# Performance work log

Hardware: AMD Instinct MI355X
Metric: run time of the kernel (lower is better)

Reference implementation:

```python
import jax, jax.numpy as jnp
import numpy as np

D_MODEL = 1024
D_FF = 4096
N_EXPERTS = 8
THRESHOLD = 0.8
EPS = 1e-6


def setup_inputs() -> dict:
    key = jax.random.key(0)
    ks = jax.random.split(key, 8)
    x = jax.random.normal(ks[0], (2, 1024, D_MODEL), jnp.float32)
    Wg = jax.random.normal(ks[1], (D_MODEL, N_EXPERTS), jnp.float32) * (D_MODEL ** -0.5)
    bg = jnp.zeros((N_EXPERTS,), jnp.float32)
    W1 = jax.random.normal(ks[2], (N_EXPERTS, D_MODEL, D_FF), jnp.float32) * (D_MODEL ** -0.5)
    b1 = jnp.zeros((N_EXPERTS, D_FF), jnp.float32)
    W3 = jax.random.normal(ks[3], (N_EXPERTS, D_MODEL, D_FF), jnp.float32) * (D_MODEL ** -0.5)
    b3 = jnp.zeros((N_EXPERTS, D_FF), jnp.float32)
    W2 = jax.random.normal(ks[4], (N_EXPERTS, D_FF, D_MODEL), jnp.float32) * (D_FF ** -0.5)
    b2 = jnp.zeros((N_EXPERTS, D_MODEL), jnp.float32)
    return {"x": x, "Wg": Wg, "bg": bg, "W1": W1, "b1": b1, "W3": W3, "b3": b3, "W2": W2, "b2": b2}


def _route(x, Wg, bg):
    # Dynamic-K (top-p) router
    logits = x @ Wg + bg                                  # [B,S,E]
    probs = jax.nn.softmax(logits, axis=-1)
    order = jnp.argsort(-probs, axis=-1)                  # descending sort indices
    sp = jnp.take_along_axis(probs, order, axis=-1)       # sorted probs
    shifted = jnp.cumsum(sp, axis=-1) - sp                # exclusive cumsum
    active = shifted < THRESHOLD
    active = active.at[..., 0].set(True)                  # always keep top-1
    ap = sp * active.astype(sp.dtype)
    aw = ap / (ap.sum(axis=-1, keepdims=True) + EPS)      # renormalized weights
    inv = jnp.argsort(order, axis=-1)                     # scatter == gather by inverse perm
    weights = jnp.take_along_axis(aw, inv, axis=-1)       # [B,S,E] in expert order
    return weights, probs, active.sum(axis=-1)


def reference(x, Wg, bg, W1, b1, W3, b3, W2, b2):
    B, S, D = x.shape
    E = W1.shape[0]
    weights, probs, active_count = _route(x, Wg, bg)
    xf = x.reshape(-1, D)                                 # [T,D]
    wf = weights.reshape(-1, E)                           # [T,E]
    # Dense grouped SwiGLU experts; zero routing weight zeroes the contribution,
    # matching the masked gather/scatter math of the original.
    h = jnp.einsum('td,edf->etf', xf, W1) + b1[:, None, :]
    g = jax.nn.silu(h) * (jnp.einsum('td,edf->etf', xf, W3) + b3[:, None, :])
    out_e = jnp.einsum('etf,efd->etd', g, W2) + b2[:, None, :]
    final = jnp.einsum('etd,te->td', out_e, wf).reshape(B, S, D)
    # auxiliary losses
    f_i = (wf > 0).astype(x.dtype).mean(axis=0)           # fraction of tokens per expert
    P_i = probs.reshape(-1, E).mean(axis=0)               # mean router prob per expert
    loss_balance = E * jnp.sum(f_i * P_i)
    loss_entropy = (-jnp.sum(probs * jnp.log(probs + EPS), axis=-1)).mean()
    return final, loss_balance, loss_entropy, active_count
```

## Files before the change

### kernel.cpp

```cpp
#include <hip/hip_runtime.h>
#include <hip/hip_bf16.h>
#include <math.h>

#define D_MODEL 1024
#define D_FF    4096
#define N_EXP   8
#define TOKENS  2048
#define THRESH  0.8f
#define EPS_R   1e-6f

#define FINAL_SIZE (TOKENS * D_MODEL)

typedef unsigned short ushort_t;
typedef __attribute__((ext_vector_type(4))) float f32x4;
typedef __attribute__((ext_vector_type(8))) short bf16x8;
typedef __attribute__((ext_vector_type(8))) unsigned short ushort8_t;

__device__ __forceinline__ unsigned short f2bf(float f) {
    unsigned u = __builtin_bit_cast(unsigned, f);
    unsigned r = (u + 0x7FFFu + ((u >> 16) & 1u)) >> 16;
    return (unsigned short)r;
}
__device__ __forceinline__ float bf2f(unsigned short b) {
    unsigned u = ((unsigned)b) << 16;
    return __builtin_bit_cast(float, u);
}

template <typename T>
__device__ __forceinline__ void gload16(const T* gsrc, T* ldst) {
    __builtin_amdgcn_global_load_lds((const __attribute__((address_space(1))) unsigned int*)gsrc,
                                     (__attribute__((address_space(3))) unsigned int*)ldst,
                                     16, 0, 0);
}

#define VMCNT4() asm volatile("s_waitcnt vmcnt(4)" ::: "memory")
#define VMCNT0() asm volatile("s_waitcnt vmcnt(0)" ::: "memory")
#define BAR()    do { __builtin_amdgcn_s_barrier(); asm volatile("" ::: "memory"); } while (0)

__global__ __launch_bounds__(256) void convert_x_kernel(const float* __restrict__ x,
                                                        ushort_t* __restrict__ xbf) {
    int i = blockIdx.x * 256 + threadIdx.x;
    const float4 v = reinterpret_cast<const float4*>(x)[i];
    ushort4 o;
    o.x = f2bf(v.x); o.y = f2bf(v.y); o.z = f2bf(v.z); o.w = f2bf(v.w);
    reinterpret_cast<ushort4*>(xbf)[i] = o;
}

__global__ __launch_bounds__(256) void wconv_all_kernel(const float* __restrict__ W1,
                                                        const float* __restrict__ W3,
                                                        const float* __restrict__ W2,
                                                        ushort_t* __restrict__ w1t,
                                                        ushort_t* __restrict__ w3t,
                                                        ushort_t* __restrict__ w2t) {
    __shared__ float sT[64][65];
    const int idx = blockIdx.x;
    const int sel = idx >> 13;
    const int r = idx & 8191;
    int K, N, k0, n0, e;
    const float* src;
    ushort_t* dst;
    if (sel < 2) {
        K = D_MODEL; N = D_FF;
        n0 = (r & 63) * 64;
        k0 = ((r >> 6) & 15) * 64;
        e = r >> 10;
        src = (sel == 0 ? W1 : W3) + (size_t)e * K * N;
        dst = (sel == 0 ? w1t : w3t) + (size_t)e * K * N;
    } else {
        K = D_FF; N = D_MODEL;
        n0 = (r & 15) * 64;
        k0 = ((r >> 4) & 63) * 64;
        e = r >> 10;
        src = W2 + (size_t)e * K * N;
        dst = w2t + (size_t)e * K * N;
    }
    const int t = threadIdx.x;
    {
        const int k = t >> 2;
        const int c = (t & 3) * 16;
        const float* s = src + (size_t)(k0 + k) * N + n0 + c;
#pragma unroll
        for (int j = 0; j < 4; ++j) {
            float4 v = *reinterpret_cast<const float4*>(s + 4 * j);
            sT[k][c + 4 * j + 0] = v.x; sT[k][c + 4 * j + 1] = v.y;
            sT[k][c + 4 * j + 2] = v.z; sT[k][c + 4 * j + 3] = v.w;
        }
    }
    __syncthreads();
    {
        const int n = t >> 2;
        const int ks = (t & 3) * 16;
        ushort_t* d = dst + (size_t)(n0 + n) * K + k0 + ks;
#pragma unroll
        for (int h = 0; h < 2; ++h) {
            ushort8_t o;
#pragma unroll
            for (int j = 0; j < 8; ++j) o[j] = f2bf(sT[ks + h * 8 + j][n]);
            *reinterpret_cast<ushort8_t*>(d + h * 8) = o;
        }
    }
}

__global__ __launch_bounds__(256) void router_kernel(const float* __restrict__ x,
                                                     const float* __restrict__ Wg,
                                                     const float* __restrict__ bg,
                                                     float* __restrict__ wts,
                                                     float* __restrict__ probs,
                                                     float* __restrict__ ent,
                                                     float* __restrict__ act_out)
{
    int wave = threadIdx.x >> 6;
    int lane = threadIdx.x & 63;
    int t = blockIdx.x * 4 + wave;

    float acc[8];
#pragma unroll
    for (int e = 0; e < 8; ++e) acc[e] = 0.f;

    const float* xrow = x + (size_t)t * D_MODEL;
    for (int d = lane; d < D_MODEL; d += 64) {
        float xv = xrow[d];
        const float4* wg = reinterpret_cast<const float4*>(Wg + (size_t)d * 8);
        float4 a = wg[0], b = wg[1];
        acc[0] += xv * a.x; acc[1] += xv * a.y; acc[2] += xv * a.z; acc[3] += xv * a.w;
        acc[4] += xv * b.x; acc[5] += xv * b.y; acc[6] += xv * b.z; acc[7] += xv * b.w;
    }
#pragma unroll
    for (int e = 0; e < 8; ++e) {
#pragma unroll
        for (int off = 32; off > 0; off >>= 1) acc[e] += __shfl_xor(acc[e], off);
    }

    if (lane == 0) {
        float l[8], p[8];
        float m = -1e30f;
#pragma unroll
        for (int e = 0; e < 8; ++e) { l[e] = acc[e] + bg[e]; m = fmaxf(m, l[e]); }
        float s = 0.f;
#pragma unroll
        for (int e = 0; e < 8; ++e) { p[e] = expf(l[e] - m); s += p[e]; }
        float inv = 1.f / s;
#pragma unroll
        for (int e = 0; e < 8; ++e) p[e] *= inv;

        int idx[8]; float sp[8];
#pragma unroll
        for (int e = 0; e < 8; ++e) { idx[e] = e; sp[e] = p[e]; }
        for (int i = 0; i < 8; ++i) {
            int best = i;
            for (int j = i + 1; j < 8; ++j) if (sp[j] > sp[best]) best = j;
            float tv = sp[i]; sp[i] = sp[best]; sp[best] = tv;
            int ti = idx[i]; idx[i] = idx[best]; idx[best] = ti;
        }
        float cum = 0.f, asum = 0.f, ap[8];
        int cnt = 0;
        for (int i = 0; i < 8; ++i) {
            int active = (i == 0) || (cum < THRESH);
            cum += sp[i];
            ap[i] = active ? sp[i] : 0.f;
            asum += ap[i];
            cnt += active;
        }
        float rinv = 1.f / (asum + EPS_R);
        float w[8];
        for (int i = 0; i < 8; ++i) w[idx[i]] = ap[i] * rinv;

        float* wrow = wts + (size_t)t * 8;
        float* prow = probs + (size_t)t * 8;
        float e_sum = 0.f;
#pragma unroll
        for (int e = 0; e < 8; ++e) {
            wrow[e] = w[e];
            prow[e] = p[e];
            e_sum -= p[e] * logf(p[e] + EPS_R);
        }
        ent[t] = e_sum;
        act_out[t] = (float)cnt;
    }
}

__global__ __launch_bounds__(512) void build_lists_kernel(const float* __restrict__ wts,
                                                          int* __restrict__ tok,
                                                          int* __restrict__ pos,
                                                          int* __restrict__ cnt) {
    const int e = threadIdx.x >> 6;
    const int lane = threadIdx.x & 63;
    int base = 0;
    for (int t0 = 0; t0 < TOKENS; t0 += 64) {
        int t = t0 + lane;
        float w = wts[(size_t)t * 8 + e];
        unsigned long long mask = __ballot(w > 0.f);
        int rank = __popcll(mask & ((1ull << lane) - 1ull));
        if (w > 0.f) {
            tok[e * TOKENS + base + rank] = t;
            pos[(size_t)t * 8 + e] = base + rank;
        } else {
            pos[(size_t)t * 8 + e] = -1;
        }
        base += __popcll(mask);
    }
    if (lane == 0) cnt[e] = base;
}

__global__ __launch_bounds__(256) void loss_kernel(const float* __restrict__ wts,
                                                   const float* __restrict__ probs,
                                                   const float* __restrict__ ent,
                                                   float* __restrict__ out_scalars)
{
    const int tid = threadIdx.x;
    const int lane = tid & 63;
    const int wv = tid >> 6;
    float fsum[8], psum[8], es = 0.f;
#pragma unroll
    for (int e = 0; e < 8; ++e) { fsum[e] = 0.f; psum[e] = 0.f; }
    for (int t = tid; t < TOKENS; t += 256) {
        const float* wrow = wts + (size_t)t * 8;
        const float* prow = probs + (size_t)t * 8;
#pragma unroll
        for (int e = 0; e < 8; ++e) {
            fsum[e] += (wrow[e] > 0.f) ? 1.f : 0.f;
            psum[e] += prow[e];
        }
        es += ent[t];
    }
#pragma unroll
    for (int e = 0; e < 8; ++e) {
#pragma unroll
        for (int off = 32; off > 0; off >>= 1) {
            fsum[e] += __shfl_xor(fsum[e], off);
            psum[e] += __shfl_xor(psum[e], off);
        }
    }
#pragma unroll
    for (int off = 32; off > 0; off >>= 1) es += __shfl_xor(es, off);

    __shared__ float red[4][17];
    if (lane == 0) {
#pragma unroll
        for (int e = 0; e < 8; ++e) { red[wv][e] = fsum[e]; red[wv][8 + e] = psum[e]; }
        red[wv][16] = es;
    }
    __syncthreads();
    if (tid == 0) {
        float tot[17];
#pragma unroll
        for (int q = 0; q < 17; ++q) tot[q] = red[0][q] + red[1][q] + red[2][q] + red[3][q];
        const float invT = 1.f / (float)TOKENS;
        float lb = 0.f;
        for (int e = 0; e < 8; ++e) lb += (tot[e] * invT) * (tot[8 + e] * invT);
        out_scalars[0] = 8.f * lb;
        out_scalars[1] = tot[16] * invT;
    }
}

__global__ __launch_bounds__(256, 2) void gemm1_kernel(const ushort_t* __restrict__ xbf,
                                                       const ushort_t* __restrict__ w1t,
                                                       const ushort_t* __restrict__ w3t,
                                                       const float* __restrict__ b1,
                                                       const float* __restrict__ b3,
                                                       const int* __restrict__ tok,
                                                       const int* __restrict__ cnts,
                                                       ushort_t* __restrict__ g,
                                                       int gbase) {
    const int z = blockIdx.z;
    const int ge = gbase + z;
    const int cnt = cnts[ge];

    const int NX = D_FF / 64;
    const int CHUNK = NX / 8;
    const int orig = blockIdx.x + NX * blockIdx.y;
    const int inner = orig >> 3;
    const int nx = (orig & 7) * CHUNK + (inner & (CHUNK - 1));
    const int ny = inner / CHUNK;
    const int m0 = ny * 128;
    const int n0 = nx * 64;
    if (m0 >= cnt) return;

    __shared__ ushort_t sA0[128 * 32], sA1[128 * 32];
    __shared__ ushort_t sB10[64 * 32], sB11[64 * 32];
    __shared__ ushort_t sB30[64 * 32], sB31[64 * 32];

    const int tid = threadIdx.x;
    const int lane = tid & 63;
    const int wave = tid >> 6;
    const int wr = wave >> 1, wc = wave & 1;

    f32x4 acc1[4][2], acc3[4][2];
#pragma unroll
    for (int i = 0; i < 4; ++i)
#pragma unroll
        for (int j = 0; j < 2; ++j) { acc1[i][j] = (f32x4)0.f; acc3[i][j] = (f32x4)0.f; }

    const int srow = tid >> 2;
    const int scol = (tid & 3) * 8;

    const ushort_t* abase[2];
#pragma unroll
    for (int r = 0; r < 2; ++r) {
        int i = m0 + srow + r * 64;
        i = (i < cnt) ? i : (cnt - 1);
        abase[r] = xbf + (size_t)tok[ge * TOKENS + i] * D_MODEL + scol;
    }
    const ushort_t* w1p = w1t + (size_t)z * D_FF * D_MODEL + (size_t)(n0 + srow) * D_MODEL + scol;
    const ushort_t* w3p = w3t + (size_t)z * D_FF * D_MODEL + (size_t)(n0 + srow) * D_MODEL + scol;

    auto stage = [&](ushort_t* dA, ushort_t* dB1, ushort_t* dB3, int kk) {
        gload16(abase[0] + kk, dA + wave * 512);
        gload16(abase[1] + kk, dA + 2048 + wave * 512);
        gload16(w1p + kk, dB1 + wave * 512);
        gload16(w3p + kk, dB3 + wave * 512);
    };
    auto compute = [&](const ushort_t* pA, const ushort_t* pB1, const ushort_t* pB3) {
        const int ko = (lane >> 4) * 8;
        const int fr = lane & 15;
        bf16x8 a[4], u1[2], u3[2];
#pragma unroll
        for (int fm = 0; fm < 4; ++fm)
            a[fm] = *reinterpret_cast<const bf16x8*>(&pA[(wr * 64 + fm * 16 + fr) * 32 + ko]);
#pragma unroll
        for (int fn = 0; fn < 2; ++fn) {
            u1[fn] = *reinterpret_cast<const bf16x8*>(&pB1[(wc * 32 + fn * 16 + fr) * 32 + ko]);
            u3[fn] = *reinterpret_cast<const bf16x8*>(&pB3[(wc * 32 + fn * 16 + fr) * 32 + ko]);
        }
#pragma unroll
        for (int fm = 0; fm < 4; ++fm)
#pragma unroll
            for (int fn = 0; fn < 2; ++fn) {
                acc1[fm][fn] = __builtin_amdgcn_mfma_f32_16x16x32_bf16(a[fm], u1[fn], acc1[fm][fn], 0, 0, 0);
                acc3[fm][fn] = __builtin_amdgcn_mfma_f32_16x16x32_bf16(a[fm], u3[fn], acc3[fm][fn], 0, 0, 0);
            }
    };

    stage(sA0, sB10, sB30, 0);
#pragma unroll 1
    for (int t = 0; t < 30; t += 2) {
        stage(sA1, sB11, sB31, (t + 1) * 32);
        VMCNT4(); BAR();
        compute(sA0, sB10, sB30);
        BAR();
        stage(sA0, sB10, sB30, (t + 2) * 32);
        VMCNT4(); BAR();
        compute(sA1, sB11, sB31);
        BAR();
    }
    stage(sA1, sB11, sB31, 31 * 32);
    VMCNT4(); BAR();
    compute(sA0, sB10, sB30);
    BAR();
    VMCNT0(); BAR();
    compute(sA1, sB11, sB31);

    ushort_t* ge_out = g + (size_t)z * TOKENS * D_FF;
#pragma unroll
    for (int fn = 0; fn < 2; ++fn) {
        int col = n0 + wc * 32 + fn * 16 + (lane & 15);
        float bb1 = b1[(size_t)ge * D_FF + col];
        float bb3 = b3[(size_t)ge * D_FF + col];
#pragma unroll
        for (int fm = 0; fm < 4; ++fm) {
#pragma unroll
            for (int r = 0; r < 4; ++r) {
                int row = m0 + wr * 64 + fm * 16 + (lane >> 4) * 4 + r;
                if (row < cnt) {
                    float h1 = acc1[fm][fn][r] + bb1;
                    float h3 = acc3[fm][fn][r] + bb3;
                    float gv = (h1 / (1.f + expf(-h1))) * h3;
                    ge_out[(size_t)row * D_FF + col] = f2bf(gv);
                }
            }
        }
    }
}

__global__ __launch_bounds__(256, 2) void gemm2_kernel(const ushort_t* __restrict__ g,
                                                       const ushort_t* __restrict__ w2t,
                                                       const float* __restrict__ b2,
                                                       const float* __restrict__ wts,
                                                       const int* __restrict__ tok,
                                                       const int* __restrict__ cnts,
                                                       ushort_t* __restrict__ part,
                                                       int gbase) {
    const int z = blockIdx.z;
    const int ge = gbase + z;
    const int cnt = cnts[ge];
    const int m0 = blockIdx.y * 128;
    if (m0 >= cnt) return;
    const int n0 = blockIdx.x * 128;

    __shared__ ushort_t sA0[128 * 32], sA1[128 * 32];
    __shared__ ushort_t sB0[128 * 32], sB1[128 * 32];

    const int tid = threadIdx.x;
    const int lane = tid & 63;
    const int wave = tid >> 6;
    const int wr = wave >> 1, wc = wave & 1;

    f32x4 acc[4][4];
#pragma unroll
    for (int i = 0; i < 4; ++i)
#pragma unroll
        for (int j = 0; j < 4; ++j) acc[i][j] = (f32x4)0.f;

    const int srow = tid >> 2;
    const int scol = (tid & 3) * 8;

    const ushort_t* ga = g + (size_t)z * TOKENS * D_FF;
    const ushort_t* ap[2];
#pragma unroll
    for (int r = 0; r < 2; ++r) {
        int i = m0 + r * 64 + srow;
        i = (i < cnt) ? i : (cnt - 1);
        ap[r] = ga + (size_t)i * D_FF + scol;
    }
    const ushort_t* w2e = w2t + (size_t)z * D_MODEL * D_FF;
    const ushort_t* bp[2];
#pragma unroll
    for (int r = 0; r < 2; ++r)
        bp[r] = w2e + (size_t)(n0 + r * 64 + srow) * D_FF + scol;

    auto stage = [&](ushort_t* dA, ushort_t* dB, int kk) {
#pragma unroll
        for (int r = 0; r < 2; ++r) {
            gload16(ap[r] + kk, dA + r * 2048 + wave * 512);
            gload16(bp[r] + kk, dB + r * 2048 + wave * 512);
        }
    };
    auto compute = [&](const ushort_t* pA, const ushort_t* pB) {
        const int ko = (lane >> 4) * 8;
        const int fr = lane & 15;
        bf16x8 a[4], b[4];
#pragma unroll
        for (int fm = 0; fm < 4; ++fm)
            a[fm] = *reinterpret_cast<const bf16x8*>(&pA[(wr * 64 + fm * 16 + fr) * 32 + ko]);
#pragma unroll
        for (int fn = 0; fn < 4; ++fn)
            b[fn] = *reinterpret_cast<const bf16x8*>(&pB[(wc * 64 + fn * 16 + fr) * 32 + ko]);
#pragma unroll
        for (int fm = 0; fm < 4; ++fm)
#pragma unroll
            for (int fn = 0; fn < 4; ++fn)
                acc[fm][fn] = __builtin_amdgcn_mfma_f32_16x16x32_bf16(a[fm], b[fn], acc[fm][fn], 0, 0, 0);
    };

    stage(sA0, sB0, 0);
#pragma unroll 1
    for (int t = 0; t < 126; t += 2) {
        stage(sA1, sB1, (t + 1) * 32);
        VMCNT4(); BAR();
        compute(sA0, sB0);
        BAR();
        stage(sA0, sB0, (t + 2) * 32);
        VMCNT4(); BAR();
        compute(sA1, sB1);
        BAR();
    }
    stage(sA1, sB1, 127 * 32);
    VMCNT4(); BAR();
    compute(sA0, sB0);
    BAR();
    VMCNT0(); BAR();
    compute(sA1, sB1);

    ushort_t* pe = part + (size_t)ge * TOKENS * D_MODEL;
#pragma unroll
    for (int fm = 0; fm < 4; ++fm) {
#pragma unroll
        for (int r = 0; r < 4; ++r) {
            int row = m0 + wr * 64 + fm * 16 + (lane >> 4) * 4 + r;
            if (row < cnt) {
                float w = wts[(size_t)tok[ge * TOKENS + row] * 8 + ge];
#pragma unroll
                for (int fn = 0; fn < 4; ++fn) {
                    int col = n0 + wc * 64 + fn * 16 + (lane & 15);
                    float bb2 = b2[(size_t)ge * D_MODEL + col];
                    pe[(size_t)row * D_MODEL + col] = f2bf((acc[fm][fn][r] + bb2) * w);
                }
            }
        }
    }
}

__global__ __launch_bounds__(256) void reduce_out_kernel(const ushort_t* __restrict__ part,
                                                         const int* __restrict__ pos,
                                                         float* __restrict__ out) {
    const int t = blockIdx.x;
    const int d = threadIdx.x;
    float4 s = make_float4(0.f, 0.f, 0.f, 0.f);
#pragma unroll
    for (int e = 0; e < 8; ++e) {
        int p = pos[(size_t)t * 8 + e];
        if (p >= 0) {
            ushort4 v = reinterpret_cast<const ushort4*>(part + ((size_t)e * TOKENS + p) * D_MODEL)[d];
            s.x += bf2f(v.x); s.y += bf2f(v.y); s.z += bf2f(v.z); s.w += bf2f(v.w);
        }
    }
    reinterpret_cast<float4*>(out + (size_t)t * D_MODEL)[d] = s;
}

extern "C" void kernel_launch(void* const* d_in, const int* in_sizes, int n_in,
                              void* d_out, int out_size, void* d_ws, size_t ws_size,
                              hipStream_t stream) {
    const float* x  = (const float*)d_in[0];
    const float* Wg = (const float*)d_in[1];
    const float* bg = (const float*)d_in[2];
    const float* W1 = (const float*)d_in[3];
    const float* b1 = (const float*)d_in[4];
    const float* W3 = (const float*)d_in[5];
    const float* b3 = (const float*)d_in[6];
    const float* W2 = (const float*)d_in[7];
    const float* b2 = (const float*)d_in[8];
    float* out = (float*)d_out;

    char* wsb = (char*)d_ws;
    ushort_t* xbf  = (ushort_t*)(wsb);
    float*    wts  = (float*)(wsb + (4u << 20));
    float*    probs= (float*)(wsb + (4u << 20) + 65536);
    float*    ent  = (float*)(wsb + (4u << 20) + 131072);
    int*      tok  = (int*)(wsb + (4u << 20) + 139264);
    int*      pos  = (int*)(wsb + (4u << 20) + 204800);
    int*      cnts = (int*)(wsb + (4u << 20) + 270336);
    ushort_t* part = (ushort_t*)(wsb + (8u << 20));

    const size_t BIG0 = (size_t)72 << 20;
    const size_t PER_E = (size_t)40 << 20;
    int GS = 8;
    if (ws_size < BIG0 + 8 * PER_E) GS = 4;
    if (ws_size < BIG0 + 4 * PER_E) GS = 2;
    if (ws_size < BIG0 + 2 * PER_E) GS = 1;

    char* big = wsb + BIG0;
    const size_t W_SZ = (size_t)GS * ((size_t)D_FF * D_MODEL * 2);
    ushort_t* w1t  = (ushort_t*)big;
    ushort_t* w3t  = (ushort_t*)(big + W_SZ);
    ushort_t* w2t  = (ushort_t*)(big + 2 * W_SZ);
    ushort_t* gbuf = (ushort_t*)(big + 3 * W_SZ);

    float* out_scalars = out + FINAL_SIZE;
    float* out_act     = out + FINAL_SIZE + 2;

    convert_x_kernel<<<TOKENS * D_MODEL / (256 * 4), 256, 0, stream>>>(x, xbf);
    router_kernel<<<TOKENS / 4, 256, 0, stream>>>(x, Wg, bg, wts, probs, ent, out_act);
    build_lists_kernel<<<1, 512, 0, stream>>>(wts, tok, pos, cnts);
    loss_kernel<<<1, 256, 0, stream>>>(wts, probs, ent, out_scalars);

    for (int g0 = 0; g0 < N_EXP; g0 += GS) {
        if (GS == 8) {
            wconv_all_kernel<<<3 * 8192, 256, 0, stream>>>(W1, W3, W2, w1t, w3t, w2t);
        } else {
            wconv_all_kernel<<<3 * 1024 * GS, 256, 0, stream>>>(
                W1 + (size_t)g0 * D_MODEL * D_FF, W3 + (size_t)g0 * D_MODEL * D_FF,
                W2 + (size_t)g0 * D_FF * D_MODEL, w1t, w3t, w2t);
        }

        gemm1_kernel<<<dim3(D_FF / 64, TOKENS / 128, GS), 256, 0, stream>>>(
            xbf, w1t, w3t, b1, b3, tok, cnts, gbuf, g0);
        gemm2_kernel<<<dim3(D_MODEL / 128, TOKENS / 128, GS), 256, 0, stream>>>(
            gbuf, w2t, b2, wts, tok, cnts, part, g0);
    }
    reduce_out_kernel<<<TOKENS, 256, 0, stream>>>(part, pos, out);
}
```

Before: 493.8 us.

## Enlarge gemm1 tiles to 256x128x64 with 8 waves and interleaved prefetch

Rewrites the fused W1/W3 SwiGLU GEMM to use 256x128 output tiles with a K step of 64, eight waves per block, and a double-buffered schedule that spreads the next stage's global-to-LDS loads between the four MFMA phases. It also raises wave priority around the MFMA bursts. The goal is more operand reuse per LDS load and better overlap of memory with compute. In exchange it uses much more LDS and registers, allows only one block per CU, and wastes more work on the ragged per-expert token counts. Separately, the non-GS==8 path now uses a per-matrix weight conversion kernel.

```diff
diff --git a/kernel.cpp b/kernel.cpp
--- a/kernel.cpp
+++ b/kernel.cpp
@@ -33,9 +33,11 @@
                                      16, 0, 0);
 }
 
+#define VMCNT2() asm volatile("s_waitcnt vmcnt(2)" ::: "memory")
 #define VMCNT4() asm volatile("s_waitcnt vmcnt(4)" ::: "memory")
 #define VMCNT0() asm volatile("s_waitcnt vmcnt(0)" ::: "memory")
 #define BAR()    do { __builtin_amdgcn_s_barrier(); asm volatile("" ::: "memory"); } while (0)
+#define MFMA(d, x, y) d = __builtin_amdgcn_mfma_f32_16x16x32_bf16(x, y, d, 0, 0, 0)
 
 __global__ __launch_bounds__(256) void convert_x_kernel(const float* __restrict__ x,
                                                         ushort_t* __restrict__ xbf) {
@@ -101,6 +103,41 @@
     }
 }
 
+__global__ __launch_bounds__(256) void wconv_kernel(const float* __restrict__ in,
+                                                    ushort_t* __restrict__ out,
+                                                    int K, int N) {
+    __shared__ float sT[64][65];
+    const int e = blockIdx.z;
+    const float* src = in + (size_t)e * K * N;
+    ushort_t* dst = out + (size_t)e * K * N;
+    const int k0 = blockIdx.y * 64, n0 = blockIdx.x * 64;
+    const int t = threadIdx.x;
+    {
+        const int k = t >> 2;
+        const int c = (t & 3) * 16;
+        const float* s = src + (size_t)(k0 + k) * N + n0 + c;
+#pragma unroll
+        for (int j = 0; j < 4; ++j) {
+            float4 v = *reinterpret_cast<const float4*>(s + 4 * j);
+            sT[k][c + 4 * j + 0] = v.x; sT[k][c + 4 * j + 1] = v.y;
+            sT[k][c + 4 * j + 2] = v.z; sT[k][c + 4 * j + 3] = v.w;
+        }
+    }
+    __syncthreads();
+    {
+        const int n = t >> 2;
+        const int ks = (t & 3) * 16;
+        ushort_t* d = dst + (size_t)(n0 + n) * K + k0 + ks;
+#pragma unroll
+        for (int h = 0; h < 2; ++h) {
+            ushort8_t o;
+#pragma unroll
+            for (int j = 0; j < 8; ++j) o[j] = f2bf(sT[ks + h * 8 + j][n]);
+            *reinterpret_cast<ushort8_t*>(d + h * 8) = o;
+        }
+    }
+}
+
 __global__ __launch_bounds__(256) void router_kernel(const float* __restrict__ x,
                                                      const float* __restrict__ Wg,
                                                      const float* __restrict__ bg,
@@ -253,7 +290,7 @@
     }
 }
 
-__global__ __launch_bounds__(256, 2) void gemm1_kernel(const ushort_t* __restrict__ xbf,
+__global__ __launch_bounds__(512, 1) void gemm1_kernel(const ushort_t* __restrict__ xbf,
                                                        const ushort_t* __restrict__ w1t,
                                                        const ushort_t* __restrict__ w3t,
                                                        const float* __restrict__ b1,
@@ -266,101 +303,168 @@
     const int ge = gbase + z;
     const int cnt = cnts[ge];
 
-    const int NX = D_FF / 64;
-    const int CHUNK = NX / 8;
+    const int NX = D_FF / 128;
     const int orig = blockIdx.x + NX * blockIdx.y;
     const int inner = orig >> 3;
-    const int nx = (orig & 7) * CHUNK + (inner & (CHUNK - 1));
-    const int ny = inner / CHUNK;
-    const int m0 = ny * 128;
-    const int n0 = nx * 64;
+    const int nx = (orig & 7) * 4 + (inner & 3);
+    const int ny = inner >> 2;
+    const int m0 = ny * 256;
+    const int n0 = nx * 128;
     if (m0 >= cnt) return;
 
-    __shared__ ushort_t sA0[128 * 32], sA1[128 * 32];
-    __shared__ ushort_t sB10[64 * 32], sB11[64 * 32];
-    __shared__ ushort_t sB30[64 * 32], sB31[64 * 32];
+    __shared__ ushort_t sA0[256 * 64], sA1[256 * 64];
+    __shared__ ushort_t sB10[128 * 64], sB11[128 * 64];
+    __shared__ ushort_t sB30[128 * 64], sB31[128 * 64];
 
     const int tid = threadIdx.x;
     const int lane = tid & 63;
     const int wave = tid >> 6;
-    const int wr = wave >> 1, wc = wave & 1;
-
-    f32x4 acc1[4][2], acc3[4][2];
-#pragma unroll
-    for (int i = 0; i < 4; ++i)
+    const int wr = wave >> 2;
+    const int wc = wave & 3;
+    const int fr = lane & 15;
+    const int ko = (lane >> 4) * 8;
+
+    f32x4 acc1[8][2], acc3[8][2];
+#pragma unroll
+    for (int i = 0; i < 8; ++i)
 #pragma unroll
         for (int j = 0; j < 2; ++j) { acc1[i][j] = (f32x4)0.f; acc3[i][j] = (f32x4)0.f; }
 
-    const int srow = tid >> 2;
-    const int scol = (tid & 3) * 8;
-
-    const ushort_t* abase[2];
+    const int srow = tid >> 3;
+    const int scol = (tid & 7) * 8;
+
+    const ushort_t* aptr[4];
+#pragma unroll
+    for (int r = 0; r < 4; ++r) {
+        int i = m0 + r * 64 + srow;
+        i = (i < cnt) ? i : (cnt - 1);
+        aptr[r] = xbf + (size_t)tok[ge * TOKENS + i] * D_MODEL + scol;
+    }
+    const ushort_t* w1e = w1t + (size_t)z * D_FF * D_MODEL;
+    const ushort_t* w3e = w3t + (size_t)z * D_FF * D_MODEL;
+    const ushort_t* b1ptr[2];
+    const ushort_t* b3ptr[2];
 #pragma unroll
     for (int r = 0; r < 2; ++r) {
-        int i = m0 + srow + r * 64;
-        i = (i < cnt) ? i : (cnt - 1);
-        abase[r] = xbf + (size_t)tok[ge * TOKENS + i] * D_MODEL + scol;
-    }
-    const ushort_t* w1p = w1t + (size_t)z * D_FF * D_MODEL + (size_t)(n0 + srow) * D_MODEL + scol;
-    const ushort_t* w3p = w3t + (size_t)z * D_FF * D_MODEL + (size_t)(n0 + srow) * D_MODEL + scol;
-
-    auto stage = [&](ushort_t* dA, ushort_t* dB1, ushort_t* dB3, int kk) {
-        gload16(abase[0] + kk, dA + wave * 512);
-        gload16(abase[1] + kk, dA + 2048 + wave * 512);
-        gload16(w1p + kk, dB1 + wave * 512);
-        gload16(w3p + kk, dB3 + wave * 512);
-    };
-    auto compute = [&](const ushort_t* pA, const ushort_t* pB1, const ushort_t* pB3) {
-        const int ko = (lane >> 4) * 8;
-        const int fr = lane & 15;
-        bf16x8 a[4], u1[2], u3[2];
-#pragma unroll
-        for (int fm = 0; fm < 4; ++fm)
-            a[fm] = *reinterpret_cast<const bf16x8*>(&pA[(wr * 64 + fm * 16 + fr) * 32 + ko]);
-#pragma unroll
-        for (int fn = 0; fn < 2; ++fn) {
-            u1[fn] = *reinterpret_cast<const bf16x8*>(&pB1[(wc * 32 + fn * 16 + fr) * 32 + ko]);
-            u3[fn] = *reinterpret_cast<const bf16x8*>(&pB3[(wc * 32 + fn * 16 + fr) * 32 + ko]);
-        }
-#pragma unroll
-        for (int fm = 0; fm < 4; ++fm)
-#pragma unroll
-            for (int fn = 0; fn < 2; ++fn) {
-                acc1[fm][fn] = __builtin_amdgcn_mfma_f32_16x16x32_bf16(a[fm], u1[fn], acc1[fm][fn], 0, 0, 0);
-                acc3[fm][fn] = __builtin_amdgcn_mfma_f32_16x16x32_bf16(a[fm], u3[fn], acc3[fm][fn], 0, 0, 0);
+        b1ptr[r] = w1e + (size_t)(n0 + r * 64 + srow) * D_MODEL + scol;
+        b3ptr[r] = w3e + (size_t)(n0 + r * 64 + srow) * D_MODEL + scol;
+    }
+    const int ldsoff = wave * 512;
+
+    {
+        const int kk = 0;
+#pragma unroll
+        for (int r = 0; r < 4; ++r) gload16(aptr[r] + kk, sA0 + r * 4096 + ldsoff);
+#pragma unroll
+        for (int r = 0; r < 2; ++r) gload16(b1ptr[r] + kk, sB10 + r * 4096 + ldsoff);
+#pragma unroll
+        for (int r = 0; r < 2; ++r) gload16(b3ptr[r] + kk, sB30 + r * 4096 + ldsoff);
+    }
+
+#pragma unroll 1
+    for (int t = 0; t < 16; ++t) {
+        const int b = t & 1;
+        const ushort_t* A   = b ? sA1  : sA0;
+        const ushort_t* B1c = b ? sB11 : sB10;
+        const ushort_t* B3c = b ? sB31 : sB30;
+        ushort_t* An  = b ? sA0  : sA1;
+        ushort_t* B1n = b ? sB10 : sB11;
+        ushort_t* B3n = b ? sB30 : sB31;
+        const bool more = (t + 1 < 16);
+        const int kk1 = (t + 1) * 64;
+
+        bf16x8 a[8];
+
+        if (more) {
+            gload16(aptr[0] + kk1, An + 0 * 4096 + ldsoff);
+            gload16(aptr[1] + kk1, An + 1 * 4096 + ldsoff);
+            VMCNT2();
+        } else {
+            VMCNT0();
+        }
+        BAR();
+#pragma unroll
+        for (int fm = 0; fm < 8; ++fm)
+            a[fm] = *reinterpret_cast<const bf16x8*>(&A[(wr * 128 + fm * 16 + fr) * 64 + ko]);
+        {
+            bf16x8 u0 = *reinterpret_cast<const bf16x8*>(&B1c[(wc * 32 + fr) * 64 + ko]);
+            bf16x8 u1 = *reinterpret_cast<const bf16x8*>(&B1c[(wc * 32 + 16 + fr) * 64 + ko]);
+            __builtin_amdgcn_s_setprio(1);
+#pragma unroll
+            for (int fm = 0; fm < 8; ++fm) {
+                MFMA(acc1[fm][0], a[fm], u0);
+                MFMA(acc1[fm][1], a[fm], u1);
             }
-    };
-
-    stage(sA0, sB10, sB30, 0);
-#pragma unroll 1
-    for (int t = 0; t < 30; t += 2) {
-        stage(sA1, sB11, sB31, (t + 1) * 32);
-        VMCNT4(); BAR();
-        compute(sA0, sB10, sB30);
+            __builtin_amdgcn_s_setprio(0);
+        }
         BAR();
-        stage(sA0, sB10, sB30, (t + 2) * 32);
-        VMCNT4(); BAR();
-        compute(sA1, sB11, sB31);
+
+        if (more) {
+            gload16(aptr[2] + kk1, An + 2 * 4096 + ldsoff);
+            gload16(aptr[3] + kk1, An + 3 * 4096 + ldsoff);
+        }
+        {
+            bf16x8 u0 = *reinterpret_cast<const bf16x8*>(&B3c[(wc * 32 + fr) * 64 + ko]);
+            bf16x8 u1 = *reinterpret_cast<const bf16x8*>(&B3c[(wc * 32 + 16 + fr) * 64 + ko]);
+            __builtin_amdgcn_s_setprio(1);
+#pragma unroll
+            for (int fm = 0; fm < 8; ++fm) {
+                MFMA(acc3[fm][0], a[fm], u0);
+                MFMA(acc3[fm][1], a[fm], u1);
+            }
+            __builtin_amdgcn_s_setprio(0);
+        }
         BAR();
-    }
-    stage(sA1, sB11, sB31, 31 * 32);
-    VMCNT4(); BAR();
-    compute(sA0, sB10, sB30);
-    BAR();
-    VMCNT0(); BAR();
-    compute(sA1, sB11, sB31);
+
+        if (more) {
+            gload16(b1ptr[0] + kk1, B1n + 0 * 4096 + ldsoff);
+            gload16(b1ptr[1] + kk1, B1n + 1 * 4096 + ldsoff);
+        }
+#pragma unroll
+        for (int fm = 0; fm < 8; ++fm)
+            a[fm] = *reinterpret_cast<const bf16x8*>(&A[(wr * 128 + fm * 16 + fr) * 64 + 32 + ko]);
+        {
+            bf16x8 u0 = *reinterpret_cast<const bf16x8*>(&B1c[(wc * 32 + fr) * 64 + 32 + ko]);
+            bf16x8 u1 = *reinterpret_cast<const bf16x8*>(&B1c[(wc * 32 + 16 + fr) * 64 + 32 + ko]);
+            __builtin_amdgcn_s_setprio(1);
+#pragma unroll
+            for (int fm = 0; fm < 8; ++fm) {
+                MFMA(acc1[fm][0], a[fm], u0);
+                MFMA(acc1[fm][1], a[fm], u1);
+            }
+            __builtin_amdgcn_s_setprio(0);
+        }
+        BAR();
+
+        if (more) {
+            gload16(b3ptr[0] + kk1, B3n + 0 * 4096 + ldsoff);
+            gload16(b3ptr[1] + kk1, B3n + 1 * 4096 + ldsoff);
+        }
+        {
+            bf16x8 u0 = *reinterpret_cast<const bf16x8*>(&B3c[(wc * 32 + fr) * 64 + 32 + ko]);
+            bf16x8 u1 = *reinterpret_cast<const bf16x8*>(&B3c[(wc * 32 + 16 + fr) * 64 + 32 + ko]);
+            __builtin_amdgcn_s_setprio(1);
+#pragma unroll
+            for (int fm = 0; fm < 8; ++fm) {
+                MFMA(acc3[fm][0], a[fm], u0);
+                MFMA(acc3[fm][1], a[fm], u1);
+            }
+            __builtin_amdgcn_s_setprio(0);
+        }
+        BAR();
+    }
 
     ushort_t* ge_out = g + (size_t)z * TOKENS * D_FF;
 #pragma unroll
     for (int fn = 0; fn < 2; ++fn) {
-        int col = n0 + wc * 32 + fn * 16 + (lane & 15);
+        int col = n0 + wc * 32 + fn * 16 + fr;
         float bb1 = b1[(size_t)ge * D_FF + col];
         float bb3 = b3[(size_t)ge * D_FF + col];
 #pragma unroll
-        for (int fm = 0; fm < 4; ++fm) {
+        for (int fm = 0; fm < 8; ++fm) {
 #pragma unroll
             for (int r = 0; r < 4; ++r) {
-                int row = m0 + wr * 64 + fm * 16 + (lane >> 4) * 4 + r;
+                int row = m0 + wr * 128 + fm * 16 + (lane >> 4) * 4 + r;
                 if (row < cnt) {
                     float h1 = acc1[fm][fn][r] + bb1;
                     float h3 = acc3[fm][fn][r] + bb3;
@@ -547,12 +651,15 @@
         if (GS == 8) {
             wconv_all_kernel<<<3 * 8192, 256, 0, stream>>>(W1, W3, W2, w1t, w3t, w2t);
         } else {
-            wconv_all_kernel<<<3 * 1024 * GS, 256, 0, stream>>>(
-                W1 + (size_t)g0 * D_MODEL * D_FF, W3 + (size_t)g0 * D_MODEL * D_FF,
-                W2 + (size_t)g0 * D_FF * D_MODEL, w1t, w3t, w2t);
-        }
-
-        gemm1_kernel<<<dim3(D_FF / 64, TOKENS / 128, GS), 256, 0, stream>>>(
+            wconv_kernel<<<dim3(D_FF / 64, D_MODEL / 64, GS), 256, 0, stream>>>(
+                W1 + (size_t)g0 * D_MODEL * D_FF, w1t, D_MODEL, D_FF);
+            wconv_kernel<<<dim3(D_FF / 64, D_MODEL / 64, GS), 256, 0, stream>>>(
+                W3 + (size_t)g0 * D_MODEL * D_FF, w3t, D_MODEL, D_FF);
+            wconv_kernel<<<dim3(D_MODEL / 64, D_FF / 64, GS), 256, 0, stream>>>(
+                W2 + (size_t)g0 * D_FF * D_MODEL, w2t, D_FF, D_MODEL);
+        }
+
+        gemm1_kernel<<<dim3(D_FF / 128, TOKENS / 256, GS), 512, 0, stream>>>(
             xbf, w1t, w3t, b1, b3, tok, cnts, gbuf, g0);
         gemm2_kernel<<<dim3(D_MODEL / 128, TOKENS / 128, GS), 256, 0, stream>>>(
             gbuf, w2t, b2, wts, tok, cnts, part, g0);
```

Result: slower. 578.9 us (+17.2%).
